# Kernel tuning notes

Measured on AMD Instinct MI355X. Metric: run time of the kernel, lower is better.

## Reference

```python
import jax, jax.numpy as jnp
import numpy as np

HIDDEN = 128
NUM_TYPES = 13
LN_EPS = 1e-5


def setup_inputs() -> dict:
    key = jax.random.key(0)
    k_adj, k_emb, k_idx, k_w, k_b = jax.random.split(key, 5)
    B, N, M, H, T = 8, 4096, 2048, HIDDEN, NUM_TYPES
    adj = jax.random.uniform(k_adj, (B, N, M), dtype=jnp.float32)
    embeds = jax.random.normal(k_emb, (B, N, H), dtype=jnp.float32)
    node_type_index = jax.random.randint(k_idx, (B, N), 0, T, dtype=jnp.int32)
    node_mask = jnp.ones((B, N), dtype=bool)
    # per-type Linear params (nn.Linear default init ~ U(-1/sqrt(H), 1/sqrt(H)))
    lim = 1.0 / np.sqrt(H)
    W = jax.random.uniform(k_w, (T, H, H), dtype=jnp.float32, minval=-lim, maxval=lim)
    b = jax.random.uniform(k_b, (T, H), dtype=jnp.float32, minval=-lim, maxval=lim)
    gamma = jnp.ones((H,), dtype=jnp.float32)
    beta = jnp.zeros((H,), dtype=jnp.float32)
    return {"adj": adj, "embeds": embeds, "node_type_index": node_type_index,
            "node_mask": node_mask, "W": W, "b": b, "gamma": gamma, "beta": beta}


def reference(adj, embeds, node_type_index, node_mask, W, b, gamma, beta):
    T = W.shape[0]
    # per-node-type linear: compute all T projections, then route by type.
    # y: [T, B, N, H]
    y = jnp.einsum('bnh,thd->tbnd', embeds, W) + b[:, None, None, :]
    onehot = jax.nn.one_hot(node_type_index, T, dtype=embeds.dtype)  # [B, N, T]
    routed = jnp.einsum('tbnd,bnt->bnd', y, onehot)                   # [B, N, H]
    x = jnp.where(node_mask[..., None], routed, embeds)
    # LayerNorm over hidden dim
    mu = jnp.mean(x, axis=-1, keepdims=True)
    var = jnp.mean(jnp.square(x - mu), axis=-1, keepdims=True)
    x = (x - mu) * jax.lax.rsqrt(var + LN_EPS) * gamma + beta
    # two-stage hypergraph aggregation: adj^T @ x, then adj @ lat
    lat = jnp.einsum('bnm,bnh->bmh', adj, x)   # [B, M, H]
    ret = jnp.einsum('bnm,bmh->bnh', adj, lat)  # [B, N, H]
    return ret
```

## Files before the change

### kernel.cpp

```cpp
#include <hip/hip_runtime.h>
#include <stdint.h>
#include <stddef.h>


typedef float    f32x4_t  __attribute__((ext_vector_type(4)));
typedef __bf16   bf16x8_t __attribute__((ext_vector_type(8)));
typedef unsigned int u32x4_t __attribute__((ext_vector_type(4)));
typedef unsigned int u32x2_t __attribute__((ext_vector_type(2)));

__device__ __forceinline__ unsigned short f2bf(float f) {
    union { float f; unsigned int u; } v; v.f = f;
    unsigned int u = v.u;
    return (unsigned short)((u + 0x7FFFu + ((u >> 16) & 1u)) >> 16);
}

__device__ __forceinline__ unsigned int cvtpk(float a, float b) {
    unsigned int r;
    asm("v_cvt_pk_bf16_f32 %0, %1, %2" : "=v"(r) : "v"(a), "v"(b));
    return r;
}

__device__ __forceinline__ bool mask_on(const unsigned char* m, int gid) {
    return (m[gid] | m[(gid >> 2) << 2]) != 0;
}

__device__ __forceinline__ int foff(int row, int g) {
    return row * 128 + (((g) ^ (row & 7)) << 4);
}

template<int GSTRIDE>
__device__ __forceinline__ void stage_B(const unsigned short* __restrict__ gb,
                                        int k0, unsigned short* ldsB, int t)
{
    const int l = t & 63, w = t >> 6;
    const int hsub = l >> 3;
    const int csrc = ((l & 7) ^ hsub) << 3;
    #pragma unroll
    for (int i = 0; i < 4; ++i) {
        const int hbase = i * 32 + w * 8;
        const unsigned short* src = gb + (size_t)(hbase + hsub) * GSTRIDE + k0 + csrc;
        unsigned short* dst = ldsB + hbase * 64;
        __builtin_amdgcn_global_load_lds(
            (__attribute__((address_space(1))) void*)src,
            (__attribute__((address_space(3))) void*)dst, 16, 0, 0);
    }
}

__global__ __launch_bounds__(256) void k0_wtrans(
    const float* __restrict__ W, unsigned short* __restrict__ WT)
{
    __shared__ float tile[128][132];
    const int t = threadIdx.x, ty = blockIdx.x;
    const float* Wt = W + (size_t)ty * 128 * 128;
    for (int it = 0; it < 16; ++it) {
        int idx = it * 256 + t;
        int h = idx >> 5, c = (idx & 31) * 4;
        *(float4*)(&tile[h][c]) = *(const float4*)(Wt + h * 128 + c);
    }
    __syncthreads();
    const int d = t >> 1, half = t & 1, h0 = half * 64;
    unsigned short* out = WT + ((size_t)ty * 128 + d) * 128 + h0;
    #pragma unroll
    for (int ch = 0; ch < 8; ++ch) {
        int h = h0 + ch * 8;
        u32x4_t o;
        o[0] = cvtpk(tile[h + 0][d], tile[h + 1][d]);
        o[1] = cvtpk(tile[h + 2][d], tile[h + 3][d]);
        o[2] = cvtpk(tile[h + 4][d], tile[h + 5][d]);
        o[3] = cvtpk(tile[h + 6][d], tile[h + 7][d]);
        *(u32x4_t*)(out + ch * 8) = o;
    }
}

__global__ __launch_bounds__(256) void k1_typed_ln(
    const float* __restrict__ embeds,
    const int*   __restrict__ ntype,
    const unsigned char* __restrict__ mask8,
    const unsigned short* __restrict__ WT,
    const float* __restrict__ bias,
    const float* __restrict__ gamma,
    const float* __restrict__ beta,
    unsigned short* __restrict__ xT)
{
    __shared__ unsigned short e_lds[64][136];
    __shared__ unsigned short y_lds[64][136];
    __shared__ unsigned short lists[13][64];
    __shared__ int cnt[13];
    __shared__ int grp_ty[32], grp_base[32], grp_n;
    __shared__ unsigned char msk[64];
    __shared__ float g_lds[128], be_lds[128];

    const int t   = threadIdx.x;
    const int bid = blockIdx.x;
    const int b   = bid & 7;
    const int n0  = (bid >> 3) << 6;
    const int gbase = b * 4096 + n0;
    const float* ebase = embeds + (size_t)gbase * 128;

    {
        const int n = t >> 2, q = t & 3;
        const float* src = ebase + n * 128 + q * 32;
        #pragma unroll
        for (int c = 0; c < 4; ++c) {
            f32x4_t va = *(const f32x4_t*)(src + c * 8);
            f32x4_t vb = *(const f32x4_t*)(src + c * 8 + 4);
            u32x4_t o;
            o[0] = cvtpk(va[0], va[1]); o[1] = cvtpk(va[2], va[3]);
            o[2] = cvtpk(vb[0], vb[1]); o[3] = cvtpk(vb[2], vb[3]);
            *(u32x4_t*)(&e_lds[n][q * 32 + c * 8]) = o;
        }
    }
    if (t < 128) { g_lds[t] = gamma[t]; be_lds[t] = beta[t]; }
    if (t < 64)  msk[t] = mask_on(mask8, gbase + t) ? 1 : 0;
    if (t < 13)  cnt[t] = 0;
    __syncthreads();

    if (t < 64) {
        int ty = ntype[(size_t)gbase + t];
        int slot = atomicAdd(&cnt[ty], 1);
        lists[ty][slot] = (unsigned short)t;
    }
    __syncthreads();
    if (t == 0) {
        int g = 0;
        for (int ty = 0; ty < 13; ++ty) {
            int c = cnt[ty];
            for (int base = 0; base < c; base += 16) {
                grp_ty[g] = ty; grp_base[g] = base; ++g;
            }
        }
        grp_n = g;
    }
    __syncthreads();

    const int NG   = grp_n;
    const int lane = t & 63, wv = t >> 6;
    const int fr = lane & 15, fg = lane >> 4;
    const int d0 = wv * 32;

    for (int g = 0; g < NG; ++g) {
        const int ty = grp_ty[g], base = grp_base[g];
        const int cend = cnt[ty] - 1;
        const int nodeA = lists[ty][min(base + fr, cend)];

        bf16x8_t afr[4];
        #pragma unroll
        for (int kk = 0; kk < 4; ++kk)
            afr[kk] = __builtin_bit_cast(bf16x8_t,
                *(const u32x4_t*)(&e_lds[nodeA][kk * 32 + fg * 8]));

        const unsigned short* wt = WT + (size_t)ty * 128 * 128;
        f32x4_t acc0 = f32x4_t{0.f, 0.f, 0.f, 0.f};
        f32x4_t acc1 = f32x4_t{0.f, 0.f, 0.f, 0.f};
        #pragma unroll
        for (int kk = 0; kk < 4; ++kk) {
            bf16x8_t b0 = __builtin_bit_cast(bf16x8_t,
                *(const u32x4_t*)(wt + (size_t)(d0 + fr) * 128 + kk * 32 + fg * 8));
            bf16x8_t b1 = __builtin_bit_cast(bf16x8_t,
                *(const u32x4_t*)(wt + (size_t)(d0 + 16 + fr) * 128 + kk * 32 + fg * 8));
            acc0 = __builtin_amdgcn_mfma_f32_16x16x32_bf16(afr[kk], b0, acc0, 0, 0, 0);
            acc1 = __builtin_amdgcn_mfma_f32_16x16x32_bf16(afr[kk], b1, acc1, 0, 0, 0);
        }

        const float bs0 = bias[ty * 128 + d0 + fr];
        const float bs1 = bias[ty * 128 + d0 + 16 + fr];
        #pragma unroll
        for (int j = 0; j < 4; ++j) {
            const int nd = lists[ty][min(base + fg * 4 + j, cend)];
            if (msk[nd]) {
                y_lds[nd][d0 + fr]      = f2bf(acc0[j] + bs0);
                y_lds[nd][d0 + 16 + fr] = f2bf(acc1[j] + bs1);
            } else {
                y_lds[nd][d0 + fr]      = e_lds[nd][d0 + fr];
                y_lds[nd][d0 + 16 + fr] = e_lds[nd][d0 + 16 + fr];
            }
        }
    }
    __syncthreads();

    for (int i = 0; i < 16; ++i) {
        const int n = wv + i * 4;
        unsigned int u = *(const unsigned int*)(&y_lds[n][lane * 2]);
        float vx = __builtin_bit_cast(float, u << 16);
        float vy = __builtin_bit_cast(float, u & 0xffff0000u);
        float s = vx + vy;
        float q = vx * vx + vy * vy;
        #pragma unroll
        for (int mw = 32; mw >= 1; mw >>= 1) {
            s += __shfl_xor(s, mw);
            q += __shfl_xor(q, mw);
        }
        const float mu  = s * 0.0078125f;
        const float var = q * 0.0078125f - mu * mu;
        const float r   = rsqrtf(var + 1e-5f);
        const float ox = (vx - mu) * r * g_lds[lane * 2]     + be_lds[lane * 2];
        const float oy = (vy - mu) * r * g_lds[lane * 2 + 1] + be_lds[lane * 2 + 1];
        *(unsigned int*)(&y_lds[n][lane * 2]) = cvtpk(ox, oy);
    }
    __syncthreads();

    const int nl = t & 63, hg = t >> 6;
    unsigned short* xrow = xT + (size_t)b * 128 * 4096 + n0 + nl;
    for (int i = 0; i < 32; ++i) {
        const int h = hg * 32 + i;
        xrow[(size_t)h * 4096] = y_lds[nl][h];
    }
}

__global__ __launch_bounds__(256) void k2_lat(
    const float* __restrict__ adj,
    const unsigned short* __restrict__ xT,
    unsigned short* __restrict__ latT)
{
    __shared__ unsigned short Al[2][32 * 64];
    __shared__ unsigned short Bl[2][128 * 64];

    const int t   = threadIdx.x;
    const int bid = blockIdx.x;
    const int b   = bid & 7;
    const int m0  = (bid >> 3) << 5;
    const float* adjb = adj + (size_t)b * 4096 * 2048;
    const unsigned short* xb = xT + (size_t)b * 128 * 4096;

    const int lane = t & 63, wv = t >> 6;
    const int wm = wv & 1, wh = wv >> 1;

    const int a_kp = t >> 3;
    const int a_m  = (t & 7) << 2;

    const int fr = lane & 15, fg = lane >> 4;
    int offA[2], offB[4][2];
    #pragma unroll
    for (int kk = 0; kk < 2; ++kk) offA[kk] = foff(wm * 16 + fr, kk * 4 + fg);
    #pragma unroll
    for (int j = 0; j < 4; ++j)
        #pragma unroll
        for (int kk = 0; kk < 2; ++kk)
            offB[j][kk] = foff(wh * 64 + j * 16 + fr, kk * 4 + fg);

    f32x4_t ar0, ar1;
    auto LOAD_A = [&](int k0) {
        const float* p = adjb + (size_t)(k0 + a_kp * 2) * 2048 + m0 + a_m;
        ar0 = *(const f32x4_t*)(p);
        ar1 = *(const f32x4_t*)(p + 2048);
    };
    auto WRITE_A = [&](int buf) {
        const int g = a_kp >> 2, wrd = a_kp & 3;
        #pragma unroll
        for (int j = 0; j < 4; ++j) {
            const int m = a_m + j;
            unsigned int pk = cvtpk(ar0[j], ar1[j]);
            *(unsigned int*)((char*)(&Al[buf][0]) + m * 128 + ((g ^ (m & 7)) << 4) + wrd * 4) = pk;
        }
    };

    f32x4_t acc[4];
    #pragma unroll
    for (int j = 0; j < 4; ++j) acc[j] = f32x4_t{0.f, 0.f, 0.f, 0.f};

    LOAD_A(0);
    stage_B<4096>(xb, 0, &Bl[0][0], t);
    WRITE_A(0);
    __syncthreads();

    for (int s = 0; s < 64; ++s) {
        const int buf = s & 1;
        if (s < 63) {
            LOAD_A((s + 1) * 64);
            stage_B<4096>(xb, (s + 1) * 64, &Bl[buf ^ 1][0], t);
        }
        bf16x8_t af[2];
        #pragma unroll
        for (int kk = 0; kk < 2; ++kk)
            af[kk] = __builtin_bit_cast(bf16x8_t,
                *(const u32x4_t*)((const char*)(&Al[buf][0]) + offA[kk]));
        #pragma unroll
        for (int j = 0; j < 4; ++j) {
            #pragma unroll
            for (int kk = 0; kk < 2; ++kk) {
                bf16x8_t bfj = __builtin_bit_cast(bf16x8_t,
                    *(const u32x4_t*)((const char*)(&Bl[buf][0]) + offB[j][kk]));
                acc[j] = __builtin_amdgcn_mfma_f32_16x16x32_bf16(af[kk], bfj, acc[j], 0, 0, 0);
            }
        }
        if (s < 63) WRITE_A(buf ^ 1);
        __syncthreads();
    }

    const int mrow = m0 + wm * 16 + (lane >> 4) * 4;
    #pragma unroll
    for (int j = 0; j < 4; ++j) {
        int col = wh * 64 + j * 16 + fr;
        unsigned int o0 = cvtpk(acc[j][0], acc[j][1]);
        unsigned int o1 = cvtpk(acc[j][2], acc[j][3]);
        unsigned int* dst = (unsigned int*)(latT + (size_t)(b * 128 + col) * 2048 + mrow);
        dst[0] = o0; dst[1] = o1;
    }
}

__global__ __launch_bounds__(256) void k3_ret(
    const float* __restrict__ adj,
    const unsigned short* __restrict__ latT,
    float* __restrict__ ret)
{
    __shared__ unsigned short Al[2][32 * 64];
    __shared__ unsigned short Bl[2][128 * 64];

    const int t   = threadIdx.x;
    const int bid = blockIdx.x;
    const int b   = bid & 7;
    const int n0  = (bid >> 3) << 5;
    const float* adjb = adj + (size_t)b * 4096 * 2048;
    const unsigned short* lb = latT + (size_t)b * 128 * 2048;

    const int lane = t & 63, wv = t >> 6;
    const int wn = wv & 1, wh = wv >> 1;

    const int a_r = t >> 3;
    const int a_c = t & 7;

    const int fr = lane & 15, fg = lane >> 4;
    int offA[2], offB[4][2];
    #pragma unroll
    for (int kk = 0; kk < 2; ++kk) offA[kk] = foff(wn * 16 + fr, kk * 4 + fg);
    #pragma unroll
    for (int j = 0; j < 4; ++j)
        #pragma unroll
        for (int kk = 0; kk < 2; ++kk)
            offB[j][kk] = foff(wh * 64 + j * 16 + fr, kk * 4 + fg);

    f32x4_t ar0, ar1;
    auto LOAD_A = [&](int k0) {
        const float* p = adjb + (size_t)(n0 + a_r) * 2048 + k0 + a_c * 8;
        ar0 = *(const f32x4_t*)(p);
        ar1 = *(const f32x4_t*)(p + 4);
    };
    auto WRITE_A = [&](int buf) {
        u32x4_t pk;
        pk[0] = cvtpk(ar0[0], ar0[1]);
        pk[1] = cvtpk(ar0[2], ar0[3]);
        pk[2] = cvtpk(ar1[0], ar1[1]);
        pk[3] = cvtpk(ar1[2], ar1[3]);
        *(u32x4_t*)((char*)(&Al[buf][0]) + a_r * 128 + ((a_c ^ (a_r & 7)) << 4)) = pk;
    };

    f32x4_t acc[4];
    #pragma unroll
    for (int j = 0; j < 4; ++j) acc[j] = f32x4_t{0.f, 0.f, 0.f, 0.f};

    LOAD_A(0);
    stage_B<2048>(lb, 0, &Bl[0][0], t);
    WRITE_A(0);
    __syncthreads();

    for (int s = 0; s < 32; ++s) {
        const int buf = s & 1;
        if (s < 31) {
            LOAD_A((s + 1) * 64);
            stage_B<2048>(lb, (s + 1) * 64, &Bl[buf ^ 1][0], t);
        }
        bf16x8_t af[2];
        #pragma unroll
        for (int kk = 0; kk < 2; ++kk)
            af[kk] = __builtin_bit_cast(bf16x8_t,
                *(const u32x4_t*)((const char*)(&Al[buf][0]) + offA[kk]));
        #pragma unroll
        for (int j = 0; j < 4; ++j) {
            #pragma unroll
            for (int kk = 0; kk < 2; ++kk) {
                bf16x8_t bfj = __builtin_bit_cast(bf16x8_t,
                    *(const u32x4_t*)((const char*)(&Bl[buf][0]) + offB[j][kk]));
                acc[j] = __builtin_amdgcn_mfma_f32_16x16x32_bf16(af[kk], bfj, acc[j], 0, 0, 0);
            }
        }
        if (s < 31) WRITE_A(buf ^ 1);
        __syncthreads();
    }

    const int nrow = n0 + wn * 16 + (lane >> 4) * 4;
    #pragma unroll
    for (int j = 0; j < 4; ++j) {
        int col = wh * 64 + j * 16 + fr;
        #pragma unroll
        for (int jj = 0; jj < 4; ++jj) {
            ret[((size_t)b * 4096 + nrow + jj) * 128 + col] = acc[j][jj];
        }
    }
}

extern "C" void kernel_launch(void* const* d_in, const int* in_sizes, int n_in,
                              void* d_out, int out_size, void* d_ws, size_t ws_size,
                              hipStream_t stream) {
    const float* adj    = (const float*)d_in[0];
    const float* embeds = (const float*)d_in[1];
    const int*   ntype  = (const int*)d_in[2];
    const unsigned char* mask8 = (const unsigned char*)d_in[3];
    const float* W      = (const float*)d_in[4];
    const float* bias   = (const float*)d_in[5];
    const float* gamma  = (const float*)d_in[6];
    const float* beta   = (const float*)d_in[7];
    float* ret = (float*)d_out;

    unsigned short* xT   = (unsigned short*)d_ws;
    unsigned short* latT = xT + (size_t)8 * 128 * 4096;
    unsigned short* WT   = latT + (size_t)8 * 128 * 2048;

    hipLaunchKernelGGL(k0_wtrans, dim3(13), dim3(256), 0, stream, W, WT);
    hipLaunchKernelGGL(k1_typed_ln, dim3(512), dim3(256), 0, stream,
                       embeds, ntype, mask8, WT, bias, gamma, beta, xT);
    hipLaunchKernelGGL(k2_lat, dim3(512), dim3(256), 0, stream, adj, xT, latT);
    hipLaunchKernelGGL(k3_ret, dim3(1024), dim3(256), 0, stream, adj, latT, ret);
}
```

Before: 167.2 us.

## Write bf16 copy of adj in k2 and stream it into k3 via LDS

While building the lat tile, k2 also writes its bf16-converted adj values to a workspace buffer. k3 then reads that bf16 copy with direct global-to-LDS loads, instead of reloading fp32 adj and converting it in registers. The aim is to halve k3's adj read and drop its conversion and LDS-write work. In exchange, k2 now writes a large extra buffer, so total HBM traffic stays about the same, and the workspace must be large enough to hold it.

```diff
diff --git a/kernel.cpp b/kernel.cpp
--- a/kernel.cpp
+++ b/kernel.cpp
@@ -44,6 +44,19 @@
             (__attribute__((address_space(1))) void*)src,
             (__attribute__((address_space(3))) void*)dst, 16, 0, 0);
     }
+}
+
+__device__ __forceinline__ void stage_A3(const unsigned short* __restrict__ ab,
+                                         int k0, unsigned short* ldsA, int t)
+{
+    const int l = t & 63, w = t >> 6;
+    const int rsub = l >> 3;
+    const int csrc = ((l & 7) ^ rsub) << 3;
+    const unsigned short* src = ab + (size_t)(w * 8 + rsub) * 2048 + k0 + csrc;
+    unsigned short* dst = ldsA + (w * 8) * 64;
+    __builtin_amdgcn_global_load_lds(
+        (__attribute__((address_space(1))) void*)src,
+        (__attribute__((address_space(3))) void*)dst, 16, 0, 0);
 }
 
 __global__ __launch_bounds__(256) void k0_wtrans(
@@ -210,7 +223,8 @@
 __global__ __launch_bounds__(256) void k2_lat(
     const float* __restrict__ adj,
     const unsigned short* __restrict__ xT,
-    unsigned short* __restrict__ latT)
+    unsigned short* __restrict__ latT,
+    unsigned short* __restrict__ adjbf)
 {
     __shared__ unsigned short Al[2][32 * 64];
     __shared__ unsigned short Bl[2][128 * 64];
@@ -221,6 +235,7 @@
     const int m0  = (bid >> 3) << 5;
     const float* adjb = adj + (size_t)b * 4096 * 2048;
     const unsigned short* xb = xT + (size_t)b * 128 * 4096;
+    unsigned short* abf = adjbf + (size_t)b * 4096 * 2048;
 
     const int lane = t & 63, wv = t >> 6;
     const int wm = wv & 1, wh = wv >> 1;
@@ -244,7 +259,7 @@
         ar0 = *(const f32x4_t*)(p);
         ar1 = *(const f32x4_t*)(p + 2048);
     };
-    auto WRITE_A = [&](int buf) {
+    auto WRITE_A = [&](int buf, int k0) {
         const int g = a_kp >> 2, wrd = a_kp & 3;
         #pragma unroll
         for (int j = 0; j < 4; ++j) {
@@ -252,6 +267,12 @@
             unsigned int pk = cvtpk(ar0[j], ar1[j]);
             *(unsigned int*)((char*)(&Al[buf][0]) + m * 128 + ((g ^ (m & 7)) << 4) + wrd * 4) = pk;
         }
+        const size_t row = (size_t)(k0 + a_kp * 2);
+        u32x2_t r0, r1;
+        r0[0] = cvtpk(ar0[0], ar0[1]); r0[1] = cvtpk(ar0[2], ar0[3]);
+        r1[0] = cvtpk(ar1[0], ar1[1]); r1[1] = cvtpk(ar1[2], ar1[3]);
+        *(u32x2_t*)(abf + row * 2048 + m0 + a_m) = r0;
+        *(u32x2_t*)(abf + (row + 1) * 2048 + m0 + a_m) = r1;
     };
 
     f32x4_t acc[4];
@@ -260,7 +281,7 @@
 
     LOAD_A(0);
     stage_B<4096>(xb, 0, &Bl[0][0], t);
-    WRITE_A(0);
+    WRITE_A(0, 0);
     __syncthreads();
 
     for (int s = 0; s < 64; ++s) {
@@ -283,7 +304,7 @@
                 acc[j] = __builtin_amdgcn_mfma_f32_16x16x32_bf16(af[kk], bfj, acc[j], 0, 0, 0);
             }
         }
-        if (s < 63) WRITE_A(buf ^ 1);
+        if (s < 63) WRITE_A(buf ^ 1, (s + 1) * 64);
         __syncthreads();
     }
 
@@ -299,7 +320,7 @@
 }
 
 __global__ __launch_bounds__(256) void k3_ret(
-    const float* __restrict__ adj,
+    const unsigned short* __restrict__ adjbf,
     const unsigned short* __restrict__ latT,
     float* __restrict__ ret)
 {
@@ -310,15 +331,12 @@
     const int bid = blockIdx.x;
     const int b   = bid & 7;
     const int n0  = (bid >> 3) << 5;
-    const float* adjb = adj + (size_t)b * 4096 * 2048;
+    const unsigned short* ab = adjbf + (size_t)b * 4096 * 2048 + (size_t)n0 * 2048;
     const unsigned short* lb = latT + (size_t)b * 128 * 2048;
 
     const int lane = t & 63, wv = t >> 6;
     const int wn = wv & 1, wh = wv >> 1;
 
-    const int a_r = t >> 3;
-    const int a_c = t & 7;
-
     const int fr = lane & 15, fg = lane >> 4;
     int offA[2], offB[4][2];
     #pragma unroll
@@ -329,34 +347,18 @@
         for (int kk = 0; kk < 2; ++kk)
             offB[j][kk] = foff(wh * 64 + j * 16 + fr, kk * 4 + fg);
 
-    f32x4_t ar0, ar1;
-    auto LOAD_A = [&](int k0) {
-        const float* p = adjb + (size_t)(n0 + a_r) * 2048 + k0 + a_c * 8;
-        ar0 = *(const f32x4_t*)(p);
-        ar1 = *(const f32x4_t*)(p + 4);
-    };
-    auto WRITE_A = [&](int buf) {
-        u32x4_t pk;
-        pk[0] = cvtpk(ar0[0], ar0[1]);
-        pk[1] = cvtpk(ar0[2], ar0[3]);
-        pk[2] = cvtpk(ar1[0], ar1[1]);
-        pk[3] = cvtpk(ar1[2], ar1[3]);
-        *(u32x4_t*)((char*)(&Al[buf][0]) + a_r * 128 + ((a_c ^ (a_r & 7)) << 4)) = pk;
-    };
-
     f32x4_t acc[4];
     #pragma unroll
     for (int j = 0; j < 4; ++j) acc[j] = f32x4_t{0.f, 0.f, 0.f, 0.f};
 
-    LOAD_A(0);
+    stage_A3(ab, 0, &Al[0][0], t);
     stage_B<2048>(lb, 0, &Bl[0][0], t);
-    WRITE_A(0);
     __syncthreads();
 
     for (int s = 0; s < 32; ++s) {
         const int buf = s & 1;
         if (s < 31) {
-            LOAD_A((s + 1) * 64);
+            stage_A3(ab, (s + 1) * 64, &Al[buf ^ 1][0], t);
             stage_B<2048>(lb, (s + 1) * 64, &Bl[buf ^ 1][0], t);
         }
         bf16x8_t af[2];
@@ -373,7 +375,6 @@
                 acc[j] = __builtin_amdgcn_mfma_f32_16x16x32_bf16(af[kk], bfj, acc[j], 0, 0, 0);
             }
         }
-        if (s < 31) WRITE_A(buf ^ 1);
         __syncthreads();
     }
 
@@ -401,13 +402,14 @@
     const float* beta   = (const float*)d_in[7];
     float* ret = (float*)d_out;
 
-    unsigned short* xT   = (unsigned short*)d_ws;
-    unsigned short* latT = xT + (size_t)8 * 128 * 4096;
-    unsigned short* WT   = latT + (size_t)8 * 128 * 2048;
+    unsigned short* xT    = (unsigned short*)d_ws;
+    unsigned short* latT  = xT + (size_t)8 * 128 * 4096;
+    unsigned short* WT    = latT + (size_t)8 * 128 * 2048;
+    unsigned short* adjbf = WT + (size_t)13 * 128 * 128;
 
     hipLaunchKernelGGL(k0_wtrans, dim3(13), dim3(256), 0, stream, W, WT);
     hipLaunchKernelGGL(k1_typed_ln, dim3(512), dim3(256), 0, stream,
                        embeds, ntype, mask8, WT, bias, gamma, beta, xT);
-    hipLaunchKernelGGL(k2_lat, dim3(512), dim3(256), 0, stream, adj, xT, latT);
-    hipLaunchKernelGGL(k3_ret, dim3(1024), dim3(256), 0, stream, adj, latT, ret);
-}
+    hipLaunchKernelGGL(k2_lat, dim3(512), dim3(256), 0, stream, adj, xT, latT, adjbf);
+    hipLaunchKernelGGL(k3_ret, dim3(1024), dim3(256), 0, stream, adjbf, latT, ret);
+}
```

Measured after the change: 192.0 us. 1.15x slower.

## Split k2 reduction over N into two chunks with separate reduce kernel

Applied to the files above, without the earlier changes.

The adj^T @ x kernel now splits the 4096-long N reduction into two halves, doubling the grid from 512 to 1024 blocks. Each block writes fp32 partial sums to a new workspace buffer. A new small kernel adds the two partials and converts them to bf16 latT. The goal is better CU occupancy on a GPU with many compute units, at the cost of extra partial-sum traffic and one more kernel launch.

```diff
diff --git a/kernel.cpp b/kernel.cpp
--- a/kernel.cpp
+++ b/kernel.cpp
@@ -210,7 +210,7 @@
 __global__ __launch_bounds__(256) void k2_lat(
     const float* __restrict__ adj,
     const unsigned short* __restrict__ xT,
-    unsigned short* __restrict__ latT)
+    float* __restrict__ pLat)
 {
     __shared__ unsigned short Al[2][32 * 64];
     __shared__ unsigned short Bl[2][128 * 64];
@@ -218,7 +218,10 @@
     const int t   = threadIdx.x;
     const int bid = blockIdx.x;
     const int b   = bid & 7;
-    const int m0  = (bid >> 3) << 5;
+    const int r   = bid >> 3;
+    const int m0  = (r & 63) << 5;
+    const int nc  = r >> 6;
+    const int nbase = nc << 11;
     const float* adjb = adj + (size_t)b * 4096 * 2048;
     const unsigned short* xb = xT + (size_t)b * 128 * 4096;
 
@@ -240,7 +243,7 @@
 
     f32x4_t ar0, ar1;
     auto LOAD_A = [&](int k0) {
-        const float* p = adjb + (size_t)(k0 + a_kp * 2) * 2048 + m0 + a_m;
+        const float* p = adjb + (size_t)(nbase + k0 + a_kp * 2) * 2048 + m0 + a_m;
         ar0 = *(const f32x4_t*)(p);
         ar1 = *(const f32x4_t*)(p + 2048);
     };
@@ -259,15 +262,15 @@
     for (int j = 0; j < 4; ++j) acc[j] = f32x4_t{0.f, 0.f, 0.f, 0.f};
 
     LOAD_A(0);
-    stage_B<4096>(xb, 0, &Bl[0][0], t);
+    stage_B<4096>(xb, nbase, &Bl[0][0], t);
     WRITE_A(0);
     __syncthreads();
 
-    for (int s = 0; s < 64; ++s) {
+    for (int s = 0; s < 32; ++s) {
         const int buf = s & 1;
-        if (s < 63) {
+        if (s < 31) {
             LOAD_A((s + 1) * 64);
-            stage_B<4096>(xb, (s + 1) * 64, &Bl[buf ^ 1][0], t);
+            stage_B<4096>(xb, nbase + (s + 1) * 64, &Bl[buf ^ 1][0], t);
         }
         bf16x8_t af[2];
         #pragma unroll
@@ -283,19 +286,30 @@
                 acc[j] = __builtin_amdgcn_mfma_f32_16x16x32_bf16(af[kk], bfj, acc[j], 0, 0, 0);
             }
         }
-        if (s < 63) WRITE_A(buf ^ 1);
+        if (s < 31) WRITE_A(buf ^ 1);
         __syncthreads();
     }
 
+    float* pb = pLat + (size_t)(nc * 8 + b) * 128 * 2048;
     const int mrow = m0 + wm * 16 + (lane >> 4) * 4;
     #pragma unroll
     for (int j = 0; j < 4; ++j) {
         int col = wh * 64 + j * 16 + fr;
-        unsigned int o0 = cvtpk(acc[j][0], acc[j][1]);
-        unsigned int o1 = cvtpk(acc[j][2], acc[j][3]);
-        unsigned int* dst = (unsigned int*)(latT + (size_t)(b * 128 + col) * 2048 + mrow);
-        dst[0] = o0; dst[1] = o1;
-    }
+        *(f32x4_t*)(pb + (size_t)col * 2048 + mrow) = acc[j];
+    }
+}
+
+__global__ __launch_bounds__(256) void k2_red(
+    const float* __restrict__ pLat,
+    unsigned short* __restrict__ latT)
+{
+    const size_t i4 = ((size_t)blockIdx.x * 256 + threadIdx.x) * 4;
+    f32x4_t s = *(const f32x4_t*)(pLat + i4);
+    s += *(const f32x4_t*)(pLat + i4 + (size_t)2097152);
+    u32x2_t o;
+    o[0] = cvtpk(s[0], s[1]);
+    o[1] = cvtpk(s[2], s[3]);
+    *(u32x2_t*)(latT + i4) = o;
 }
 
 __global__ __launch_bounds__(256) void k3_ret(
@@ -404,10 +418,12 @@
     unsigned short* xT   = (unsigned short*)d_ws;
     unsigned short* latT = xT + (size_t)8 * 128 * 4096;
     unsigned short* WT   = latT + (size_t)8 * 128 * 2048;
+    float* pLat = (float*)(WT + (size_t)13 * 128 * 128);
 
     hipLaunchKernelGGL(k0_wtrans, dim3(13), dim3(256), 0, stream, W, WT);
     hipLaunchKernelGGL(k1_typed_ln, dim3(512), dim3(256), 0, stream,
                        embeds, ntype, mask8, WT, bias, gamma, beta, xT);
-    hipLaunchKernelGGL(k2_lat, dim3(512), dim3(256), 0, stream, adj, xT, latT);
+    hipLaunchKernelGGL(k2_lat, dim3(1024), dim3(256), 0, stream, adj, xT, pLat);
+    hipLaunchKernelGGL(k2_red, dim3(2048), dim3(256), 0, stream, pLat, latT);
     hipLaunchKernelGGL(k3_ret, dim3(1024), dim3(256), 0, stream, adj, latT, ret);
 }
```

Measured after the change: 186.5 us. 11.5% more time.
